# Kernel tuning notes

Hardware: AMD Instinct MI355X
Metric: run time of the kernel (lower is better)

## Reference

```python
import jax, jax.numpy as jnp
import numpy as np

N = 50000
E = 300000
D_IN = 256
D_OUT = 256


def setup_inputs() -> dict:
    key = jax.random.key(0)
    ks = jax.random.split(key, 9)
    obj_vecs = jax.random.normal(ks[0], (N, D_IN), dtype=jnp.float32)
    rel_vecs = jax.random.normal(ks[1], (N, D_IN), dtype=jnp.float32)
    edge_index = jax.random.randint(ks[2], (E, 2), 0, N, dtype=jnp.int64)
    s = 1.0 / np.sqrt(D_IN)
    # SAGEConv params: lin_l (applied to aggregated neighbors, with bias),
    # lin_r (applied to root/self features, no bias). One pair per conv.
    W_l_obj = jax.random.uniform(ks[3], (D_OUT, D_IN), minval=-s, maxval=s, dtype=jnp.float32)
    b_l_obj = jax.random.uniform(ks[4], (D_OUT,), minval=-s, maxval=s, dtype=jnp.float32)
    W_r_obj = jax.random.uniform(ks[5], (D_OUT, D_IN), minval=-s, maxval=s, dtype=jnp.float32)
    W_l_rel = jax.random.uniform(ks[6], (D_OUT, D_IN), minval=-s, maxval=s, dtype=jnp.float32)
    b_l_rel = jax.random.uniform(ks[7], (D_OUT,), minval=-s, maxval=s, dtype=jnp.float32)
    W_r_rel = jax.random.uniform(ks[8], (D_OUT, D_IN), minval=-s, maxval=s, dtype=jnp.float32)
    return {"obj_vecs": obj_vecs, "rel_vecs": rel_vecs, "edge_index": edge_index,
            "W_l_obj": W_l_obj, "b_l_obj": b_l_obj, "W_r_obj": W_r_obj,
            "W_l_rel": W_l_rel, "b_l_rel": b_l_rel, "W_r_rel": W_r_rel}


def _sage_conv(x, src, dst, W_l, b_l, W_r):
    # mean aggregation of source-node features at destination nodes
    msg = x[src]                                             # [E, D_IN] gather
    summed = jax.ops.segment_sum(msg, dst, num_segments=N)   # [N, D_IN]
    cnt = jax.ops.segment_sum(jnp.ones((src.shape[0],), x.dtype), dst, num_segments=N)
    agg = summed / jnp.maximum(cnt, 1.0)[:, None]
    # out = lin_l(agg) + lin_r(x)
    return agg @ W_l.T + b_l + x @ W_r.T


def reference(obj_vecs, rel_vecs, edge_index,
              W_l_obj, b_l_obj, W_r_obj, W_l_rel, b_l_rel, W_r_rel):
    # module transposes [E,2] -> [2,E]; PyG: messages flow src=row0 -> dst=row1
    src = edge_index[:, 0]
    dst = edge_index[:, 1]
    obj_out = _sage_conv(obj_vecs, src, dst, W_l_obj, b_l_obj, W_r_obj)
    rel_out = _sage_conv(rel_vecs, src, dst, W_l_rel, b_l_rel, W_r_rel)
    return (obj_out, rel_out)
```

## Files before the change

kernel.cpp:

```cpp
#include <hip/hip_runtime.h>

#define N_NODES 50000
#define N_EDGES 300000
#define DFEAT 256
#define KCAT 512
#define MT 16
#define APAD 8
#define AROW (KCAT + APAD)
#define NWELEM (KCAT * DFEAT)
#define CAP 32

typedef __attribute__((ext_vector_type(8))) short bf16x8;
typedef __attribute__((ext_vector_type(4))) float f32x4;

__device__ __forceinline__ unsigned short f2bf(float f) {
    union { float f; unsigned int u; } c; c.f = f;
    unsigned int r = c.u + 0x7FFF + ((c.u >> 16) & 1);
    return (unsigned short)(r >> 16);
}

__global__ void k_prep(const float* __restrict__ Wl_o, const float* __restrict__ Wr_o,
                       const float* __restrict__ Wl_r, const float* __restrict__ Wr_r,
                       unsigned short* __restrict__ Wb_o, unsigned short* __restrict__ Wb_r,
                       int* __restrict__ cnt) {
    int id = blockIdx.x * blockDim.x + threadIdx.x;
    int wid  = id & (NWELEM - 1);
    int j    = wid & 7;
    int lane = (wid >> 3) & 63;
    int frag = wid >> 9;
    int nt   = frag & 15;
    int kb   = frag >> 4;
    int k = kb * 32 + (lane >> 4) * 8 + j;
    int n = nt * 16 + (lane & 15);
    if (id < NWELEM) {
        float v = (k < 256) ? Wl_o[n * 256 + k] : Wr_o[n * 256 + (k - 256)];
        Wb_o[wid] = f2bf(v);
    } else {
        float v = (k < 256) ? Wl_r[n * 256 + k] : Wr_r[n * 256 + (k - 256)];
        Wb_r[wid] = f2bf(v);
    }
    if (id < N_NODES) cnt[id] = 0;
}

__global__ void k_place(const long long* __restrict__ ei, int* __restrict__ cnt,
                        int* __restrict__ srcs2, int E) {
    int e = blockIdx.x * blockDim.x + threadIdx.x;
    if (e < E) {
        long long v = __builtin_nontemporal_load(&ei[e]);
        int s = (int)(v & 0xffffffffLL);
        int d = (int)(v >> 32);
        if ((unsigned)d < (unsigned)N_NODES) {
            int r = atomicAdd(&cnt[d], 1);
            if (r < CAP)
                srcs2[d * CAP + r] = ((unsigned)s < (unsigned)N_NODES) ? s : 0;
        }
    }
}

__global__ __launch_bounds__(256, 8)
void k_fused(const float* __restrict__ x_obj, const float* __restrict__ x_rel,
             const unsigned short* __restrict__ Wb_obj, const unsigned short* __restrict__ Wb_rel,
             const float* __restrict__ b_obj, const float* __restrict__ b_rel,
             const int* __restrict__ cnt, const int* __restrict__ srcs2,
             float* __restrict__ out, int n) {
    __shared__ unsigned short A[MT][AROW];

    const int tz = blockIdx.y;
    const float* __restrict__ x   = tz ? x_rel  : x_obj;
    const unsigned short* __restrict__ Wb = tz ? Wb_rel : Wb_obj;
    const float* __restrict__ bia = tz ? b_rel  : b_obj;
    float* __restrict__ outp = out + (size_t)tz * (size_t)N_NODES * DFEAT;

    const int t = threadIdx.x;
    const int wave = t >> 6, lane = t & 63;
    const int node0 = blockIdx.x * MT;

    const float4* __restrict__ x4 = (const float4*)x;
    for (int il = wave; il < MT; il += 4) {
        int node = node0 + il;
        float4 accv = make_float4(0.f, 0.f, 0.f, 0.f);
        float4 xv   = make_float4(0.f, 0.f, 0.f, 0.f);
        if (node < n) {
            xv = x4[(size_t)node * 64 + lane];
            int ecraw = cnt[node];
            if (ecraw < 0) ecraw = 0;
            int ec = (ecraw < CAP) ? ecraw : CAP;
            const int* __restrict__ sp = srcs2 + node * CAP;
            int e = 0;
            for (; e + 3 < ec; e += 4) {
                unsigned s0 = (unsigned)sp[e],     s1 = (unsigned)sp[e + 1];
                unsigned s2 = (unsigned)sp[e + 2], s3 = (unsigned)sp[e + 3];
                if (s0 >= (unsigned)n) s0 = 0;
                if (s1 >= (unsigned)n) s1 = 0;
                if (s2 >= (unsigned)n) s2 = 0;
                if (s3 >= (unsigned)n) s3 = 0;
                float4 v0 = x4[(size_t)s0 * 64 + lane];
                float4 v1 = x4[(size_t)s1 * 64 + lane];
                float4 v2 = x4[(size_t)s2 * 64 + lane];
                float4 v3 = x4[(size_t)s3 * 64 + lane];
                accv.x += (v0.x + v1.x) + (v2.x + v3.x);
                accv.y += (v0.y + v1.y) + (v2.y + v3.y);
                accv.z += (v0.z + v1.z) + (v2.z + v3.z);
                accv.w += (v0.w + v1.w) + (v2.w + v3.w);
            }
            if (e + 1 < ec) {
                unsigned s0 = (unsigned)sp[e], s1 = (unsigned)sp[e + 1];
                if (s0 >= (unsigned)n) s0 = 0;
                if (s1 >= (unsigned)n) s1 = 0;
                float4 v0 = x4[(size_t)s0 * 64 + lane];
                float4 v1 = x4[(size_t)s1 * 64 + lane];
                accv.x += v0.x + v1.x; accv.y += v0.y + v1.y;
                accv.z += v0.z + v1.z; accv.w += v0.w + v1.w;
                e += 2;
            }
            if (e < ec) {
                unsigned s0 = (unsigned)sp[e];
                if (s0 >= (unsigned)n) s0 = 0;
                float4 v = x4[(size_t)s0 * 64 + lane];
                accv.x += v.x; accv.y += v.y; accv.z += v.z; accv.w += v.w;
            }
            float c = (float)ecraw;
            float inv = 1.0f / fmaxf(c, 1.0f);
            accv.x *= inv; accv.y *= inv; accv.z *= inv; accv.w *= inv;
        }
        ushort4 a16 = make_ushort4(f2bf(accv.x), f2bf(accv.y), f2bf(accv.z), f2bf(accv.w));
        ushort4 x16 = make_ushort4(f2bf(xv.x),  f2bf(xv.y),  f2bf(xv.z),  f2bf(xv.w));
        *(ushort4*)&A[il][4 * lane]       = a16;
        *(ushort4*)&A[il][256 + 4 * lane] = x16;
    }
    __syncthreads();

    const int nt0 = wave * 4;
    const int lq  = lane >> 4;
    const int lm  = lane & 15;

    f32x4 acc[4];
    #pragma unroll
    for (int ct = 0; ct < 4; ct++) {
        float b = bia[(nt0 + ct) * 16 + lm];
        acc[ct] = (f32x4){b, b, b, b};
    }

    const bf16x8* __restrict__ Wb8 = (const bf16x8*)Wb;
    #pragma unroll
    for (int kb = 0; kb < 16; kb++) {
        bf16x8 af = *(const bf16x8*)&A[lm][kb * 32 + lq * 8];
        #pragma unroll
        for (int ct = 0; ct < 4; ct++) {
            bf16x8 bf = Wb8[(size_t)(kb * 16 + nt0 + ct) * 64 + lane];
            acc[ct] = __builtin_amdgcn_mfma_f32_16x16x32_bf16(af, bf, acc[ct], 0, 0, 0);
        }
    }

    #pragma unroll
    for (int ct = 0; ct < 4; ct++) {
        int col = (nt0 + ct) * 16 + lm;
        #pragma unroll
        for (int r = 0; r < 4; r++) {
            int node = node0 + lq * 4 + r;
            if (node < n)
                __builtin_nontemporal_store(acc[ct][r], &outp[((size_t)node << 8) + col]);
        }
    }
}

extern "C" void kernel_launch(void* const* d_in, const int* in_sizes, int n_in,
                              void* d_out, int out_size, void* d_ws, size_t ws_size,
                              hipStream_t stream) {
    const float*     obj  = (const float*)d_in[0];
    const float*     rel  = (const float*)d_in[1];
    const long long* ei   = (const long long*)d_in[2];
    const float*     Wl_o = (const float*)d_in[3];
    const float*     bl_o = (const float*)d_in[4];
    const float*     Wr_o = (const float*)d_in[5];
    const float*     Wl_r = (const float*)d_in[6];
    const float*     bl_r = (const float*)d_in[7];
    const float*     Wr_r = (const float*)d_in[8];
    float* out = (float*)d_out;

    char* w = (char*)d_ws;
    size_t o = 0;
    auto alloc = [&](size_t b) { size_t r = o; o += (b + 255) & ~(size_t)255; return r; };
    int*            cnt    = (int*)(w + alloc((size_t)N_NODES * 4));
    int*            srcs2  = (int*)(w + alloc((size_t)N_NODES * CAP * 4));
    unsigned short* Wb_o   = (unsigned short*)(w + alloc((size_t)NWELEM * 2));
    unsigned short* Wb_r   = (unsigned short*)(w + alloc((size_t)NWELEM * 2));

    k_prep<<<(2 * NWELEM) / 256, 256, 0, stream>>>(Wl_o, Wr_o, Wl_r, Wr_r, Wb_o, Wb_r, cnt);
    k_place<<<(N_EDGES + 255) / 256, 256, 0, stream>>>(ei, cnt, srcs2, N_EDGES);

    dim3 g((N_NODES + MT - 1) / MT, 2);
    k_fused<<<g, 256, 0, stream>>>(obj, rel, Wb_o, Wb_r, bl_o, bl_r, cnt, srcs2, out, N_NODES);
}
```

Baseline: 311.6 us.

## Pre-cast node features to bf16 so the neighbor gather reads half the bytes

Adds a kernel that converts both feature matrices to bf16 up front. The fused kernel then gathers bf16 rows and writes the self features straight into shared memory without converting them. This is meant to cut gather memory traffic, at the cost of an extra full pass over the inputs and summing neighbours from rounded values. It also drops the redundant source clamping and replaces the nontemporal output stores with plain stores.

```diff
diff --git a/kernel.cpp b/kernel.cpp
--- a/kernel.cpp
+++ b/kernel.cpp
@@ -9,6 +9,7 @@
 #define AROW (KCAT + APAD)
 #define NWELEM (KCAT * DFEAT)
 #define CAP 32
+#define XQ4 ((N_NODES * DFEAT) / 8)
 
 typedef __attribute__((ext_vector_type(8))) short bf16x8;
 typedef __attribute__((ext_vector_type(4))) float f32x4;
@@ -19,10 +20,30 @@
     return (unsigned short)(r >> 16);
 }
 
+__device__ __forceinline__ float bf2f(unsigned short u) {
+    union { unsigned int i; float f; } c; c.i = (unsigned)u << 16; return c.f;
+}
+
+__global__ void k_xcast(const float* __restrict__ xo, const float* __restrict__ xr,
+                        unsigned short* __restrict__ xbo, unsigned short* __restrict__ xbr,
+                        int* __restrict__ cnt) {
+    int id = blockIdx.x * blockDim.x + threadIdx.x;
+    const float4* __restrict__ src;
+    unsigned short* __restrict__ dst;
+    int k;
+    if (id < XQ4) { src = (const float4*)xo; dst = xbo; k = id; }
+    else          { src = (const float4*)xr; dst = xbr; k = id - XQ4; }
+    float4 a = src[2 * k], b = src[2 * k + 1];
+    ushort4 u0 = make_ushort4(f2bf(a.x), f2bf(a.y), f2bf(a.z), f2bf(a.w));
+    ushort4 u1 = make_ushort4(f2bf(b.x), f2bf(b.y), f2bf(b.z), f2bf(b.w));
+    *(ushort4*)&dst[8 * k]     = u0;
+    *(ushort4*)&dst[8 * k + 4] = u1;
+    if (id < N_NODES) cnt[id] = 0;
+}
+
 __global__ void k_prep(const float* __restrict__ Wl_o, const float* __restrict__ Wr_o,
                        const float* __restrict__ Wl_r, const float* __restrict__ Wr_r,
-                       unsigned short* __restrict__ Wb_o, unsigned short* __restrict__ Wb_r,
-                       int* __restrict__ cnt) {
+                       unsigned short* __restrict__ Wb_o, unsigned short* __restrict__ Wb_r) {
     int id = blockIdx.x * blockDim.x + threadIdx.x;
     int wid  = id & (NWELEM - 1);
     int j    = wid & 7;
@@ -39,7 +60,6 @@
         float v = (k < 256) ? Wl_r[n * 256 + k] : Wr_r[n * 256 + (k - 256)];
         Wb_r[wid] = f2bf(v);
     }
-    if (id < N_NODES) cnt[id] = 0;
 }
 
 __global__ void k_place(const long long* __restrict__ ei, int* __restrict__ cnt,
@@ -58,7 +78,7 @@
 }
 
 __global__ __launch_bounds__(256, 8)
-void k_fused(const float* __restrict__ x_obj, const float* __restrict__ x_rel,
+void k_fused(const unsigned short* __restrict__ xb_obj, const unsigned short* __restrict__ xb_rel,
              const unsigned short* __restrict__ Wb_obj, const unsigned short* __restrict__ Wb_rel,
              const float* __restrict__ b_obj, const float* __restrict__ b_rel,
              const int* __restrict__ cnt, const int* __restrict__ srcs2,
@@ -66,67 +86,59 @@
     __shared__ unsigned short A[MT][AROW];
 
     const int tz = blockIdx.y;
-    const float* __restrict__ x   = tz ? x_rel  : x_obj;
+    const unsigned short* __restrict__ xb = tz ? xb_rel : xb_obj;
     const unsigned short* __restrict__ Wb = tz ? Wb_rel : Wb_obj;
-    const float* __restrict__ bia = tz ? b_rel  : b_obj;
+    const float* __restrict__ bia = tz ? b_rel : b_obj;
     float* __restrict__ outp = out + (size_t)tz * (size_t)N_NODES * DFEAT;
 
     const int t = threadIdx.x;
     const int wave = t >> 6, lane = t & 63;
     const int node0 = blockIdx.x * MT;
 
-    const float4* __restrict__ x4 = (const float4*)x;
+    const ushort4* __restrict__ xb4 = (const ushort4*)xb;
     for (int il = wave; il < MT; il += 4) {
         int node = node0 + il;
-        float4 accv = make_float4(0.f, 0.f, 0.f, 0.f);
-        float4 xv   = make_float4(0.f, 0.f, 0.f, 0.f);
+        float ax = 0.f, ay = 0.f, az = 0.f, aw = 0.f;
+        ushort4 xv = make_ushort4(0, 0, 0, 0);
+        float c = 0.f;
         if (node < n) {
-            xv = x4[(size_t)node * 64 + lane];
+            xv = xb4[(size_t)node * 64 + lane];
             int ecraw = cnt[node];
             if (ecraw < 0) ecraw = 0;
             int ec = (ecraw < CAP) ? ecraw : CAP;
+            c = (float)ecraw;
             const int* __restrict__ sp = srcs2 + node * CAP;
             int e = 0;
             for (; e + 3 < ec; e += 4) {
-                unsigned s0 = (unsigned)sp[e],     s1 = (unsigned)sp[e + 1];
-                unsigned s2 = (unsigned)sp[e + 2], s3 = (unsigned)sp[e + 3];
-                if (s0 >= (unsigned)n) s0 = 0;
-                if (s1 >= (unsigned)n) s1 = 0;
-                if (s2 >= (unsigned)n) s2 = 0;
-                if (s3 >= (unsigned)n) s3 = 0;
-                float4 v0 = x4[(size_t)s0 * 64 + lane];
-                float4 v1 = x4[(size_t)s1 * 64 + lane];
-                float4 v2 = x4[(size_t)s2 * 64 + lane];
-                float4 v3 = x4[(size_t)s3 * 64 + lane];
-                accv.x += (v0.x + v1.x) + (v2.x + v3.x);
-                accv.y += (v0.y + v1.y) + (v2.y + v3.y);
-                accv.z += (v0.z + v1.z) + (v2.z + v3.z);
-                accv.w += (v0.w + v1.w) + (v2.w + v3.w);
+                int s0 = sp[e], s1 = sp[e + 1], s2 = sp[e + 2], s3 = sp[e + 3];
+                ushort4 v0 = xb4[(size_t)s0 * 64 + lane];
+                ushort4 v1 = xb4[(size_t)s1 * 64 + lane];
+                ushort4 v2 = xb4[(size_t)s2 * 64 + lane];
+                ushort4 v3 = xb4[(size_t)s3 * 64 + lane];
+                ax += (bf2f(v0.x) + bf2f(v1.x)) + (bf2f(v2.x) + bf2f(v3.x));
+                ay += (bf2f(v0.y) + bf2f(v1.y)) + (bf2f(v2.y) + bf2f(v3.y));
+                az += (bf2f(v0.z) + bf2f(v1.z)) + (bf2f(v2.z) + bf2f(v3.z));
+                aw += (bf2f(v0.w) + bf2f(v1.w)) + (bf2f(v2.w) + bf2f(v3.w));
             }
             if (e + 1 < ec) {
-                unsigned s0 = (unsigned)sp[e], s1 = (unsigned)sp[e + 1];
-                if (s0 >= (unsigned)n) s0 = 0;
-                if (s1 >= (unsigned)n) s1 = 0;
-                float4 v0 = x4[(size_t)s0 * 64 + lane];
-                float4 v1 = x4[(size_t)s1 * 64 + lane];
-                accv.x += v0.x + v1.x; accv.y += v0.y + v1.y;
-                accv.z += v0.z + v1.z; accv.w += v0.w + v1.w;
+                int s0 = sp[e], s1 = sp[e + 1];
+                ushort4 v0 = xb4[(size_t)s0 * 64 + lane];
+                ushort4 v1 = xb4[(size_t)s1 * 64 + lane];
+                ax += bf2f(v0.x) + bf2f(v1.x); ay += bf2f(v0.y) + bf2f(v1.y);
+                az += bf2f(v0.z) + bf2f(v1.z); aw += bf2f(v0.w) + bf2f(v1.w);
                 e += 2;
             }
             if (e < ec) {
-                unsigned s0 = (unsigned)sp[e];
-                if (s0 >= (unsigned)n) s0 = 0;
-                float4 v = x4[(size_t)s0 * 64 + lane];
-                accv.x += v.x; accv.y += v.y; accv.z += v.z; accv.w += v.w;
+                int s0 = sp[e];
+                ushort4 v = xb4[(size_t)s0 * 64 + lane];
+                ax += bf2f(v.x); ay += bf2f(v.y); az += bf2f(v.z); aw += bf2f(v.w);
             }
-            float c = (float)ecraw;
             float inv = 1.0f / fmaxf(c, 1.0f);
-            accv.x *= inv; accv.y *= inv; accv.z *= inv; accv.w *= inv;
-        }
-        ushort4 a16 = make_ushort4(f2bf(accv.x), f2bf(accv.y), f2bf(accv.z), f2bf(accv.w));
-        ushort4 x16 = make_ushort4(f2bf(xv.x),  f2bf(xv.y),  f2bf(xv.z),  f2bf(xv.w));
+            ax *= inv; ay *= inv; az *= inv; aw *= inv;
+        }
+        ushort4 a16 = make_ushort4(f2bf(ax), f2bf(ay), f2bf(az), f2bf(aw));
         *(ushort4*)&A[il][4 * lane]       = a16;
-        *(ushort4*)&A[il][256 + 4 * lane] = x16;
+        *(ushort4*)&A[il][256 + 4 * lane] = xv;
     }
     __syncthreads();
 
@@ -158,8 +170,7 @@
         #pragma unroll
         for (int r = 0; r < 4; r++) {
             int node = node0 + lq * 4 + r;
-            if (node < n)
-                __builtin_nontemporal_store(acc[ct][r], &outp[((size_t)node << 8) + col]);
+            if (node < n) outp[((size_t)node << 8) + col] = acc[ct][r];
         }
     }
 }
@@ -185,10 +196,13 @@
     int*            srcs2  = (int*)(w + alloc((size_t)N_NODES * CAP * 4));
     unsigned short* Wb_o   = (unsigned short*)(w + alloc((size_t)NWELEM * 2));
     unsigned short* Wb_r   = (unsigned short*)(w + alloc((size_t)NWELEM * 2));
-
-    k_prep<<<(2 * NWELEM) / 256, 256, 0, stream>>>(Wl_o, Wr_o, Wl_r, Wr_r, Wb_o, Wb_r, cnt);
+    unsigned short* xb_o   = (unsigned short*)(w + alloc((size_t)N_NODES * DFEAT * 2));
+    unsigned short* xb_r   = (unsigned short*)(w + alloc((size_t)N_NODES * DFEAT * 2));
+
+    k_xcast<<<(2 * XQ4 + 255) / 256, 256, 0, stream>>>(obj, rel, xb_o, xb_r, cnt);
+    k_prep<<<(2 * NWELEM) / 256, 256, 0, stream>>>(Wl_o, Wr_o, Wl_r, Wr_r, Wb_o, Wb_r);
     k_place<<<(N_EDGES + 255) / 256, 256, 0, stream>>>(ei, cnt, srcs2, N_EDGES);
 
     dim3 g((N_NODES + MT - 1) / MT, 2);
-    k_fused<<<g, 256, 0, stream>>>(obj, rel, Wb_o, Wb_r, bl_o, bl_r, cnt, srcs2, out, N_NODES);
-}
+    k_fused<<<g, 256, 0, stream>>>(xb_o, xb_r, Wb_o, Wb_r, bl_o, bl_r, cnt, srcs2, out, N_NODES);
+}
```

After: 309.6 us. About the same (-0.7%).
